# Performance work log

Measured on AMD Instinct MI355X. Metric: run time of the kernel, lower is better.

## Reference

```python
import jax, jax.numpy as jnp
import numpy as np

B, N, F_IN, F_OUT = 8, 2048, 64, 64
ALPHA = 0.2  # LeakyReLU negative slope


def setup_inputs() -> dict:
    key = jax.random.key(0)
    k1, k2, k3 = jax.random.split(key, 3)
    h = jax.random.normal(k1, (B, N, F_IN), dtype=jnp.float32)
    # xavier_uniform-like scale for params
    lim_w = np.sqrt(6.0 / (F_IN + F_OUT)).astype(np.float32)
    W = jax.random.uniform(k2, (F_IN, F_OUT), minval=-lim_w, maxval=lim_w, dtype=jnp.float32)
    lim_a = np.sqrt(6.0 / (2 * F_OUT + 1)).astype(np.float32)
    a = jax.random.uniform(k3, (2 * F_OUT, 1), minval=-lim_a, maxval=lim_a, dtype=jnp.float32)
    return {"h": h, "W": W, "a": a}


def reference(h, W, a):
    # Wh: [B, N, F_out]
    Wh = jnp.einsum("bnf,fo->bno", h, W)
    # Decompose concat([Wh_i, Wh_j]) @ a  ==  Wh_i @ a_src + Wh_j @ a_dst
    a_src = a[:F_OUT, 0]   # [F_out]
    a_dst = a[F_OUT:, 0]   # [F_out]
    s_src = Wh @ a_src     # [B, N]
    s_dst = Wh @ a_dst     # [B, N]
    e = s_src[:, :, None] + s_dst[:, None, :]          # [B, N, N]
    e = jnp.where(e > 0, e, ALPHA * e)                 # LeakyReLU
    attention = jax.nn.softmax(e, axis=2)              # softmax over j
    # dropout is identity in eval mode (training=False)
    h_prime = jnp.einsum("bij,bjo->bio", attention, Wh)
    return jax.nn.elu(h_prime)
```

## Files before the change

kernel.cpp:

```cpp
#include <hip/hip_runtime.h>
#include <math.h>


#define B 8
#define N 2048
#define F 64
#define NROW (B * N)
#define NKP 2052
#define ST 65

__device__ __forceinline__ unsigned int ord32(float v) {
  unsigned int u = __float_as_uint(v);
  return (u & 0x80000000u) ? ~u : (u | 0x80000000u);
}

__global__ __launch_bounds__(256) void k_wh(const float* __restrict__ h,
                                            const float* __restrict__ W,
                                            const float* __restrict__ a,
                                            float* __restrict__ Wh,
                                            float* __restrict__ c,
                                            float* __restrict__ d) {
  __shared__ float hl[1024];
  int t = threadIdx.x, lane = t & 63, wid = t >> 6;
  int blk = blockIdx.x;
  *(float4*)&hl[t * 4] = *(const float4*)&h[(size_t)blk * 1024 + t * 4];
  float wreg[64];
#pragma unroll
  for (int k = 0; k < 64; ++k) wreg[k] = W[k * 64 + lane];
  float as = a[lane], ad = a[64 + lane];
  __syncthreads();
#pragma unroll
  for (int rr = 0; rr < 4; ++rr) {
    int rl = wid * 4 + rr;
    int row = blk * 16 + rl;
    float acc = 0.f;
#pragma unroll
    for (int kk = 0; kk < 16; ++kk) {
      float4 hq = *(const float4*)&hl[rl * 64 + kk * 4];
      acc = fmaf(hq.x, wreg[kk * 4 + 0], acc);
      acc = fmaf(hq.y, wreg[kk * 4 + 1], acc);
      acc = fmaf(hq.z, wreg[kk * 4 + 2], acc);
      acc = fmaf(hq.w, wreg[kk * 4 + 3], acc);
    }
    Wh[(size_t)row * 64 + lane] = acc;
    float ps = acc * as, pd = acc * ad;
#pragma unroll
    for (int off = 32; off > 0; off >>= 1) {
      ps += __shfl_xor(ps, off, 64);
      pd += __shfl_xor(pd, off, 64);
    }
    if (lane == 0) { c[row] = ps; d[row] = pd; }
  }
}

__global__ __launch_bounds__(256) void k_rank(const float* __restrict__ d,
                                              const float* __restrict__ c,
                                              float* __restrict__ E1,
                                              float* __restrict__ E2,
                                              int* __restrict__ perm,
                                              int* __restrict__ kidx,
                                              float* __restrict__ M) {
  int t = threadIdx.x, lane = t & 63, wid = t >> 6;
  int row = blockIdx.x * 4 + wid;
  int b = row >> 11, j = row & (N - 1);
  const float* db = d + b * N;
  float dj = db[j];
  float thr = -c[row];
  unsigned long long kj = ((unsigned long long)ord32(dj) << 11) | (unsigned)j;
  int cnt = 0, cnt2 = 0;
  float m = -INFINITY;
#pragma unroll 8
  for (int it = 0; it < N / 64; ++it) {
    int jj = it * 64 + lane;
    float v = db[jj];
    unsigned long long kv = ((unsigned long long)ord32(v) << 11) | (unsigned)jj;
    cnt  += (kv < kj) ? 1 : 0;
    cnt2 += (v <= thr) ? 1 : 0;
    m = fmaxf(m, v);
  }
#pragma unroll
  for (int off = 32; off > 0; off >>= 1) {
    cnt  += __shfl_xor(cnt,  off, 64);
    cnt2 += __shfl_xor(cnt2, off, 64);
    m = fmaxf(m, __shfl_xor(m, off, 64));
  }
  if (lane == 0) {
    int r = b * N + cnt;
    E1[r]   = __expf(dj - m);
    E2[r]   = __expf(0.2f * (dj - m));
    perm[r] = j;
    kidx[row] = cnt2;
    if (j == 0) M[b] = m;
  }
}

__global__ __launch_bounds__(256) void k_scan(const float* __restrict__ Wh,
                                              const int* __restrict__ perm,
                                              const float* __restrict__ E1,
                                              const float* __restrict__ E2,
                                              float* __restrict__ Suf,
                                              float* __restrict__ Pre) {
  __shared__ float wt1[4], wt2[4];
  int o = blockIdx.x, b = blockIdx.y;
  int t = threadIdx.x, lane = t & 63, wid = t >> 6;
  int r0 = t * 8;
  const float* Whb = Wh + (size_t)b * N * 64;
  const int* pb = perm + b * N;
  const float* e1 = E1 + b * N;
  const float* e2 = E2 + b * N;
  float x1[8], x2[8];
#pragma unroll
  for (int q = 0; q < 8; ++q) {
    int r = r0 + q;
    float val = 1.0f;
    if (o < 64) val = Whb[(size_t)pb[r] * 64 + o];
    x1[q] = e1[r] * val;
    x2[q] = e2[r] * val;
  }
  float lp[8], ss[8];
  float s2 = 0.f;
#pragma unroll
  for (int q = 0; q < 8; ++q) { s2 += x2[q]; lp[q] = s2; }
  float s1 = 0.f;
#pragma unroll
  for (int q = 7; q >= 0; --q) { s1 += x1[q]; ss[q] = s1; }
  float i2 = s2;
#pragma unroll
  for (int off = 1; off < 64; off <<= 1) {
    float v = __shfl_up(i2, off, 64);
    if (lane >= off) i2 += v;
  }
  float r1 = s1;
#pragma unroll
  for (int off = 1; off < 64; off <<= 1) {
    float v = __shfl_down(r1, off, 64);
    if (lane < 64 - off) r1 += v;
  }
  if (lane == 63) wt2[wid] = i2;
  if (lane == 0)  wt1[wid] = r1;
  __syncthreads();
  float base2 = 0.f, after1 = 0.f, tot2 = 0.f;
#pragma unroll
  for (int w = 0; w < 4; ++w) {
    float a2 = wt2[w], a1 = wt1[w];
    tot2 += a2;
    if (w < wid) base2 += a2;
    if (w > wid) after1 += a1;
  }
  float excl = base2 + (i2 - s2);
  float aftr = after1 + (r1 - s1);
  float* Sb = Suf + ((size_t)b * ST + o) * NKP;
  float* Pb = Pre + ((size_t)b * ST + o) * NKP;
  float4 sv0 = { aftr + ss[0], aftr + ss[1], aftr + ss[2], aftr + ss[3] };
  float4 sv1 = { aftr + ss[4], aftr + ss[5], aftr + ss[6], aftr + ss[7] };
  float4 pv0 = { excl, excl + lp[0], excl + lp[1], excl + lp[2] };
  float4 pv1 = { excl + lp[3], excl + lp[4], excl + lp[5], excl + lp[6] };
  *(float4*)&Sb[r0]     = sv0;
  *(float4*)&Sb[r0 + 4] = sv1;
  *(float4*)&Pb[r0]     = pv0;
  *(float4*)&Pb[r0 + 4] = pv1;
  if (t == 255) { Sb[N] = 0.f; Pb[N] = tot2; }
}

__global__ __launch_bounds__(256) void k_final(const float* __restrict__ c,
                                               const float* __restrict__ M,
                                               const int* __restrict__ kidx,
                                               const float* __restrict__ Suf,
                                               const float* __restrict__ Pre,
                                               float* __restrict__ out) {
  int t = threadIdx.x, lane = t & 63, wid = t >> 6;
  int row = blockIdx.x * 4 + wid;
  int b = row >> 11;
  int k = kidx[row];
  float cpM = c[row] + M[b];
  float f1, f2;
  if (cpM > 0.f) { f1 = 1.f;                 f2 = __expf(-0.8f * cpM); }
  else           { f1 = __expf(0.8f * cpM);  f2 = 1.f; }
  size_t basev = ((size_t)b * ST + lane) * NKP + k;
  size_t based = ((size_t)b * ST + 64)   * NKP + k;
  float S  = Suf[basev], P  = Pre[basev];
  float Sd = Suf[based], Pd = Pre[based];
  float v = (f1 * S + f2 * P) / (f1 * Sd + f2 * Pd);
  out[(size_t)row * 64 + lane] = (v > 0.f) ? v : expm1f(v);
}

extern "C" void kernel_launch(void* const* d_in, const int* in_sizes, int n_in,
                              void* d_out, int out_size, void* d_ws, size_t ws_size,
                              hipStream_t stream) {
  (void)in_sizes; (void)n_in; (void)out_size; (void)ws_size;
  const float* h = (const float*)d_in[0];
  const float* W = (const float*)d_in[1];
  const float* a = (const float*)d_in[2];
  float* out = (float*)d_out;

  float* ws = (float*)d_ws;
  size_t off = 0;
  float* Wh   = ws + off; off += (size_t)NROW * F;
  float* c    = ws + off; off += NROW;
  float* d    = ws + off; off += NROW;
  float* E1   = ws + off; off += NROW;
  float* E2   = ws + off; off += NROW;
  float* M    = ws + off; off += 16;
  int*   perm = (int*)(ws + off); off += NROW;
  int*   kidx = (int*)(ws + off); off += NROW;
  float* Suf  = ws + off; off += (size_t)B * ST * NKP;
  float* Pre  = ws + off; off += (size_t)B * ST * NKP;

  k_wh   <<<NROW / 16, 256, 0, stream>>>(h, W, a, Wh, c, d);
  k_rank <<<NROW / 4,  256, 0, stream>>>(d, c, E1, E2, perm, kidx, M);
  k_scan <<<dim3(ST, B), 256, 0, stream>>>(Wh, perm, E1, E2, Suf, Pre);
  k_final<<<NROW / 4,  256, 0, stream>>>(c, M, kidx, Suf, Pre, out);
}
```

Before: 110.0 us.

## Split prefix-scan into chunked two-pass scan with row-major Suf/Pre layout

Replaces the single scan kernel, which had one block per (feature, batch) doing strided gathers, with two kernels. The first gathers the permuted Wh rows with coalesced float4 loads, scales them by E1/E2, writes Y1/Y2 and per-chunk totals. The second does per-chunk prefix and suffix scans plus cross-chunk offsets. Suf/Pre become [b][k][feature] with an 80-float stride, so k_final reads contiguous values per row instead of 64 strided ones. This costs an extra launch, extra Y1/Y2 global traffic, and a serial loop over chunk totals in every thread.

```diff
diff --git a/kernel.cpp b/kernel.cpp
--- a/kernel.cpp
+++ b/kernel.cpp
@@ -6,8 +6,10 @@
 #define N 2048
 #define F 64
 #define NROW (B * N)
-#define NKP 2052
-#define ST 65
+#define NK (N + 1)
+#define STP 80
+#define CHK 64
+#define NCH (N / CHK)
 
 __device__ __forceinline__ unsigned int ord32(float v) {
   unsigned int u = __float_as_uint(v);
@@ -94,72 +96,152 @@
   }
 }
 
-__global__ __launch_bounds__(256) void k_scan(const float* __restrict__ Wh,
-                                              const int* __restrict__ perm,
-                                              const float* __restrict__ E1,
-                                              const float* __restrict__ E2,
-                                              float* __restrict__ Suf,
-                                              float* __restrict__ Pre) {
-  __shared__ float wt1[4], wt2[4];
-  int o = blockIdx.x, b = blockIdx.y;
-  int t = threadIdx.x, lane = t & 63, wid = t >> 6;
-  int r0 = t * 8;
-  const float* Whb = Wh + (size_t)b * N * 64;
-  const int* pb = perm + b * N;
-  const float* e1 = E1 + b * N;
-  const float* e2 = E2 + b * N;
-  float x1[8], x2[8];
-#pragma unroll
-  for (int q = 0; q < 8; ++q) {
-    int r = r0 + q;
-    float val = 1.0f;
-    if (o < 64) val = Whb[(size_t)pb[r] * 64 + o];
-    x1[q] = e1[r] * val;
-    x2[q] = e2[r] * val;
-  }
-  float lp[8], ss[8];
-  float s2 = 0.f;
-#pragma unroll
-  for (int q = 0; q < 8; ++q) { s2 += x2[q]; lp[q] = s2; }
-  float s1 = 0.f;
-#pragma unroll
-  for (int q = 7; q >= 0; --q) { s1 += x1[q]; ss[q] = s1; }
-  float i2 = s2;
-#pragma unroll
-  for (int off = 1; off < 64; off <<= 1) {
-    float v = __shfl_up(i2, off, 64);
-    if (lane >= off) i2 += v;
-  }
-  float r1 = s1;
-#pragma unroll
-  for (int off = 1; off < 64; off <<= 1) {
-    float v = __shfl_down(r1, off, 64);
-    if (lane < 64 - off) r1 += v;
-  }
-  if (lane == 63) wt2[wid] = i2;
-  if (lane == 0)  wt1[wid] = r1;
+__global__ __launch_bounds__(256) void k_permE(const float* __restrict__ Wh,
+                                               const int* __restrict__ perm,
+                                               const float* __restrict__ E1,
+                                               const float* __restrict__ E2,
+                                               float* __restrict__ Y1,
+                                               float* __restrict__ Y2,
+                                               float* __restrict__ T1,
+                                               float* __restrict__ T2,
+                                               float* __restrict__ Td1,
+                                               float* __restrict__ Td2) {
+  __shared__ float part1[4][64], part2[4][64];
+  int chunk = blockIdx.x, b = blockIdx.y;
+  int t = threadIdx.x, lane = t & 63, w = t >> 6;
+  int rl = t >> 2, q = t & 3;
+  int gr = b * N + chunk * CHK + rl;
+  int p = perm[gr];
+  float e1 = E1[gr], e2 = E2[gr];
+  const float4* src = (const float4*)(Wh + ((size_t)b * N + p) * 64 + q * 16);
+  float4* y1p = (float4*)(Y1 + (size_t)gr * 64 + q * 16);
+  float4* y2p = (float4*)(Y2 + (size_t)gr * 64 + q * 16);
+  float a1[16], a2[16];
+#pragma unroll
+  for (int i = 0; i < 4; ++i) {
+    float4 v = src[i];
+    float4 w1 = { v.x * e1, v.y * e1, v.z * e1, v.w * e1 };
+    float4 w2 = { v.x * e2, v.y * e2, v.z * e2, v.w * e2 };
+    y1p[i] = w1; y2p[i] = w2;
+    a1[i * 4 + 0] = w1.x; a1[i * 4 + 1] = w1.y; a1[i * 4 + 2] = w1.z; a1[i * 4 + 3] = w1.w;
+    a2[i * 4 + 0] = w2.x; a2[i * 4 + 1] = w2.y; a2[i * 4 + 2] = w2.z; a2[i * 4 + 3] = w2.w;
+  }
+#pragma unroll
+  for (int cix = 0; cix < 16; ++cix) {
+    float v1 = a1[cix], v2 = a2[cix];
+#pragma unroll
+    for (int off = 4; off < 64; off <<= 1) {
+      v1 += __shfl_xor(v1, off, 64);
+      v2 += __shfl_xor(v2, off, 64);
+    }
+    a1[cix] = v1; a2[cix] = v2;
+  }
+  if (lane < 4) {
+#pragma unroll
+    for (int cix = 0; cix < 16; ++cix) {
+      part1[w][lane * 16 + cix] = a1[cix];
+      part2[w][lane * 16 + cix] = a2[cix];
+    }
+  }
   __syncthreads();
-  float base2 = 0.f, after1 = 0.f, tot2 = 0.f;
-#pragma unroll
-  for (int w = 0; w < 4; ++w) {
-    float a2 = wt2[w], a1 = wt1[w];
-    tot2 += a2;
-    if (w < wid) base2 += a2;
-    if (w > wid) after1 += a1;
-  }
-  float excl = base2 + (i2 - s2);
-  float aftr = after1 + (r1 - s1);
-  float* Sb = Suf + ((size_t)b * ST + o) * NKP;
-  float* Pb = Pre + ((size_t)b * ST + o) * NKP;
-  float4 sv0 = { aftr + ss[0], aftr + ss[1], aftr + ss[2], aftr + ss[3] };
-  float4 sv1 = { aftr + ss[4], aftr + ss[5], aftr + ss[6], aftr + ss[7] };
-  float4 pv0 = { excl, excl + lp[0], excl + lp[1], excl + lp[2] };
-  float4 pv1 = { excl + lp[3], excl + lp[4], excl + lp[5], excl + lp[6] };
-  *(float4*)&Sb[r0]     = sv0;
-  *(float4*)&Sb[r0 + 4] = sv1;
-  *(float4*)&Pb[r0]     = pv0;
-  *(float4*)&Pb[r0 + 4] = pv1;
-  if (t == 255) { Sb[N] = 0.f; Pb[N] = tot2; }
+  if (t < 64) {
+    float s1 = part1[0][t] + part1[1][t] + part1[2][t] + part1[3][t];
+    float s2 = part2[0][t] + part2[1][t] + part2[2][t] + part2[3][t];
+    T1[((size_t)b * NCH + chunk) * 64 + t] = s1;
+    T2[((size_t)b * NCH + chunk) * 64 + t] = s2;
+  }
+  if (t >= 64 && t < 128) {
+    int lr = t - 64;
+    float v1 = E1[b * N + chunk * CHK + lr];
+    float v2 = E2[b * N + chunk * CHK + lr];
+#pragma unroll
+    for (int off = 1; off < 64; off <<= 1) {
+      v1 += __shfl_xor(v1, off, 64);
+      v2 += __shfl_xor(v2, off, 64);
+    }
+    if (lr == 0) { Td1[b * NCH + chunk] = v1; Td2[b * NCH + chunk] = v2; }
+  }
+}
+
+__global__ __launch_bounds__(256) void k_scan2(const float* __restrict__ Y1,
+                                               const float* __restrict__ Y2,
+                                               const float* __restrict__ E1,
+                                               const float* __restrict__ E2,
+                                               const float* __restrict__ T1,
+                                               const float* __restrict__ T2,
+                                               const float* __restrict__ Td1,
+                                               const float* __restrict__ Td2,
+                                               float* __restrict__ Suf,
+                                               float* __restrict__ Pre) {
+  __shared__ float wt1[4][64], wt2[4][64];
+  int chunk = blockIdx.x, b = blockIdx.y;
+  int t = threadIdx.x, o = t & 63, w = t >> 6;
+  int cb = chunk * CHK;
+  size_t ybase = ((size_t)b * N + cb + w * 16) * 64 + o;
+  float pex[16]; float run2 = 0.f;
+#pragma unroll
+  for (int i = 0; i < 16; ++i) { pex[i] = run2; run2 += Y2[ybase + (size_t)i * 64]; }
+  float sin_[16]; float run1 = 0.f;
+#pragma unroll
+  for (int i = 15; i >= 0; --i) { run1 += Y1[ybase + (size_t)i * 64]; sin_[i] = run1; }
+  wt2[w][o] = run2; wt1[w][o] = run1;
+  __syncthreads();
+  float bw2 = 0.f, aw1 = 0.f, allw2 = 0.f;
+#pragma unroll
+  for (int w2 = 0; w2 < 4; ++w2) {
+    float v2 = wt2[w2][o];
+    allw2 += v2;
+    if (w2 < w) bw2 += v2;
+    if (w2 > w) aw1 += wt1[w2][o];
+  }
+  float bc2 = 0.f, ac1 = 0.f;
+  for (int cc = 0; cc < NCH; ++cc) {
+    float t2v = T2[((size_t)b * NCH + cc) * 64 + o];
+    float t1v = T1[((size_t)b * NCH + cc) * 64 + o];
+    if (cc < chunk) bc2 += t2v;
+    if (cc > chunk) ac1 += t1v;
+  }
+  float base2 = bc2 + bw2, after1 = ac1 + aw1;
+  size_t obase = ((size_t)b * NK + cb + w * 16) * STP + o;
+#pragma unroll
+  for (int i = 0; i < 16; ++i) {
+    Pre[obase + (size_t)i * STP] = base2 + pex[i];
+    Suf[obase + (size_t)i * STP] = after1 + sin_[i];
+  }
+  if (chunk == NCH - 1 && w == 3) {
+    Pre[((size_t)b * NK + N) * STP + o] = bc2 + allw2;
+    Suf[((size_t)b * NK + N) * STP + o] = 0.f;
+  }
+  if (w == 0) {
+    int lr = o;
+    int gr = b * N + cb + lr;
+    float e1 = E1[gr], e2 = E2[gr];
+    float ip2 = e2;
+#pragma unroll
+    for (int off = 1; off < 64; off <<= 1) {
+      float v = __shfl_up(ip2, off, 64);
+      if (lr >= off) ip2 += v;
+    }
+    float is1 = e1;
+#pragma unroll
+    for (int off = 1; off < 64; off <<= 1) {
+      float v = __shfl_down(is1, off, 64);
+      if (lr < 64 - off) is1 += v;
+    }
+    float db2 = 0.f, da1 = 0.f;
+    for (int cc = 0; cc < NCH; ++cc) {
+      float v2 = Td2[b * NCH + cc], v1 = Td1[b * NCH + cc];
+      if (cc < chunk) db2 += v2;
+      if (cc > chunk) da1 += v1;
+    }
+    size_t kb = ((size_t)b * NK + cb + lr) * STP + 64;
+    Pre[kb] = db2 + (ip2 - e2);
+    Suf[kb] = da1 + is1;
+    if (chunk == NCH - 1 && lr == 63) {
+      Pre[((size_t)b * NK + N) * STP + 64] = db2 + ip2;
+      Suf[((size_t)b * NK + N) * STP + 64] = 0.f;
+    }
+  }
 }
 
 __global__ __launch_bounds__(256) void k_final(const float* __restrict__ c,
@@ -176,10 +258,9 @@
   float f1, f2;
   if (cpM > 0.f) { f1 = 1.f;                 f2 = __expf(-0.8f * cpM); }
   else           { f1 = __expf(0.8f * cpM);  f2 = 1.f; }
-  size_t basev = ((size_t)b * ST + lane) * NKP + k;
-  size_t based = ((size_t)b * ST + 64)   * NKP + k;
-  float S  = Suf[basev], P  = Pre[basev];
-  float Sd = Suf[based], Pd = Pre[based];
+  size_t base = ((size_t)b * NK + k) * STP;
+  float S  = Suf[base + lane], P  = Pre[base + lane];
+  float Sd = Suf[base + 64],   Pd = Pre[base + 64];
   float v = (f1 * S + f2 * P) / (f1 * Sd + f2 * Pd);
   out[(size_t)row * 64 + lane] = (v > 0.f) ? v : expm1f(v);
 }
@@ -203,11 +284,18 @@
   float* M    = ws + off; off += 16;
   int*   perm = (int*)(ws + off); off += NROW;
   int*   kidx = (int*)(ws + off); off += NROW;
-  float* Suf  = ws + off; off += (size_t)B * ST * NKP;
-  float* Pre  = ws + off; off += (size_t)B * ST * NKP;
+  float* Y1   = ws + off; off += (size_t)NROW * F;
+  float* Y2   = ws + off; off += (size_t)NROW * F;
+  float* T1   = ws + off; off += (size_t)B * NCH * 64;
+  float* T2   = ws + off; off += (size_t)B * NCH * 64;
+  float* Td1  = ws + off; off += (size_t)B * NCH;
+  float* Td2  = ws + off; off += (size_t)B * NCH;
+  float* Suf  = ws + off; off += (size_t)B * NK * STP;
+  float* Pre  = ws + off; off += (size_t)B * NK * STP;
 
   k_wh   <<<NROW / 16, 256, 0, stream>>>(h, W, a, Wh, c, d);
   k_rank <<<NROW / 4,  256, 0, stream>>>(d, c, E1, E2, perm, kidx, M);
-  k_scan <<<dim3(ST, B), 256, 0, stream>>>(Wh, perm, E1, E2, Suf, Pre);
+  k_permE<<<dim3(NCH, B), 256, 0, stream>>>(Wh, perm, E1, E2, Y1, Y2, T1, T2, Td1, Td2);
+  k_scan2<<<dim3(NCH, B), 256, 0, stream>>>(Y1, Y2, E1, E2, T1, T2, Td1, Td2, Suf, Pre);
   k_final<<<NROW / 4,  256, 0, stream>>>(c, M, kidx, Suf, Pre, out);
 }
```

After: 110.0 us. Within noise of the previous version (+0.0%).
